# Kernel tuning notes

Measured on AMD Instinct MI355X. Metric: run time of the kernel, lower is better.

## Reference

```python
import jax, jax.numpy as jnp
import numpy as np

B, S, H = 32, 2048, 1024


def setup_inputs() -> dict:
    key = jax.random.key(0)
    k1, k2, k3, k4, k5, k6 = jax.random.split(key, 6)
    hidden = jax.random.normal(k1, (B, H), dtype=jnp.float32)
    encoder_outputs = jax.random.normal(k2, (B, S, H), dtype=jnp.float32)
    lengths = jax.random.randint(k3, (B,), 1, S + 1, dtype=jnp.int64)
    scale = 1.0 / np.sqrt(H)
    Wq = jax.random.normal(k4, (H, H), dtype=jnp.float32) * scale
    Wk = jax.random.normal(k5, (H, H), dtype=jnp.float32) * scale
    v = jax.random.uniform(k6, (H,), dtype=jnp.float32)  # torch.rand init
    return {"hidden": hidden, "encoder_outputs": encoder_outputs,
            "lengths": lengths, "Wq": Wq, "Wk": Wk, "v": v}


def reference(hidden, encoder_outputs, lengths, Wq, Wk, v):
    # query: (B, 1, H); nn.Linear(bias=False) applies x @ W.T
    query = (hidden @ Wq.T)[:, None, :]
    keys = jnp.einsum('bsh,kh->bsk', encoder_outputs, Wk)  # (B, S, H)
    energy = jnp.tanh(query + keys)                         # (B, S, H)
    attn = jnp.einsum('bsh,h->bs', energy, v)               # (B, S)
    seq = encoder_outputs.shape[1]
    mask = jnp.arange(seq)[None, :] < lengths[:, None]      # (B, S)
    attn = jnp.where(mask, attn, -jnp.inf)
    return jax.nn.softmax(attn, axis=1)
```

## Files before the change

kernel.cpp:

```cpp
#include <hip/hip_runtime.h>
#include <hip/hip_fp16.h>
#include <stdint.h>

#define B_SZ 32
#define S_SZ 2048
#define H_SZ 1024
#define M_SZ (B_SZ * S_SZ)

typedef _Float16 half8 __attribute__((ext_vector_type(8)));
typedef float floatx4 __attribute__((ext_vector_type(4)));

struct h4 { _Float16 x, y, z, w; };

__global__ __launch_bounds__(256) void convert_f32_to_f16(
    const float* __restrict__ in, h4* __restrict__ out, int n4) {
  int i = blockIdx.x * blockDim.x + threadIdx.x;
  int stride = gridDim.x * blockDim.x;
  const float4* in4 = (const float4*)in;
  for (; i < n4; i += stride) {
    float4 f = in4[i];
    h4 o;
    o.x = (_Float16)f.x; o.y = (_Float16)f.y;
    o.z = (_Float16)f.z; o.w = (_Float16)f.w;
    out[i] = o;
  }
}

__global__ __launch_bounds__(256) void query_kernel(
    const float* __restrict__ hidden, const float* __restrict__ Wq,
    float* __restrict__ q) {
  int t = blockIdx.x * blockDim.x + threadIdx.x;
  int b = t & 31;
  int n = t >> 5;
  const float4* h4p = (const float4*)(hidden + (size_t)b * H_SZ);
  const float4* w4p = (const float4*)(Wq + (size_t)n * H_SZ);
  float acc = 0.f;
  #pragma unroll 4
  for (int i = 0; i < H_SZ / 4; ++i) {
    float4 h = h4p[i], w = w4p[i];
    acc = fmaf(h.x, w.x, acc);
    acc = fmaf(h.y, w.y, acc);
    acc = fmaf(h.z, w.z, acc);
    acc = fmaf(h.w, w.w, acc);
  }
  q[(size_t)b * H_SZ + n] = acc;
}

__device__ __forceinline__ void gl_lds16(const void* g, void* l) {
  __builtin_amdgcn_global_load_lds(
      (const __attribute__((address_space(1))) void*)g,
      (__attribute__((address_space(3))) void*)l,
      16, 0, 0);
}

__device__ __forceinline__ float fast_tanh(float x) {
  float ax = fabsf(x);
  float e = __expf(ax * -2.0f);
  float t = (1.0f - e) / (1.0f + e);
  return copysignf(t, x);
}

#define TILE 128
#define BK 32

__global__ __launch_bounds__(256) void fused_keys_kernel(
    const _Float16* __restrict__ A,
    const _Float16* __restrict__ Bt,
    const float* __restrict__ q,
    const float* __restrict__ v,
    float* __restrict__ partial)
{
  __shared__ _Float16 As[TILE * BK];
  __shared__ _Float16 Bs[TILE * BK];
  __shared__ float rowsum[TILE];
  __shared__ float q_l[TILE];
  __shared__ float v_l[TILE];

  const int tid  = threadIdx.x;
  const int w    = tid >> 6;
  const int lane = tid & 63;
  const int bm   = blockIdx.x >> 3;
  const int bn   = blockIdx.x & 7;
  const int R0   = bm * TILE;
  const int C0   = bn * TILE;
  const int bidx = R0 >> 11;

  if (tid < TILE) {
    q_l[tid] = q[(size_t)bidx * H_SZ + C0 + tid];
    v_l[tid] = v[C0 + tid];
    rowsum[tid] = 0.f;
  }

  const int wm = w >> 1, wn = w & 1;
  const int cL = lane & 15, quad = lane >> 4;

  floatx4 acc[4][4];
  #pragma unroll
  for (int m = 0; m < 4; ++m)
    #pragma unroll
    for (int n = 0; n < 4; ++n)
      acc[m][n] = (floatx4){0.f, 0.f, 0.f, 0.f};

  const int srow   = lane >> 2;
  const int schunk = lane & 3;

  const _Float16* Ablk = A + (size_t)R0 * H_SZ;
  const _Float16* Bblk = Bt + (size_t)C0 * H_SZ;

  for (int kt = 0; kt < H_SZ / BK; ++kt) {
    __syncthreads();
    const int kof = kt * BK;
    #pragma unroll
    for (int r = 0; r < 2; ++r) {
      const int row = w * 16 + r * 64 + srow;
      const int ldsbase = (w * 16 + r * 64) * (BK * 2);
      gl_lds16(Ablk + (size_t)row * H_SZ + kof + schunk * 8, (char*)As + ldsbase);
      gl_lds16(Bblk + (size_t)row * H_SZ + kof + schunk * 8, (char*)Bs + ldsbase);
    }
    __syncthreads();

    half8 af[4], bf[4];
    #pragma unroll
    for (int m = 0; m < 4; ++m)
      af[m] = *(const half8*)(As + (wm * 64 + m * 16 + cL) * BK + quad * 8);
    #pragma unroll
    for (int n = 0; n < 4; ++n)
      bf[n] = *(const half8*)(Bs + (wn * 64 + n * 16 + cL) * BK + quad * 8);
    #pragma unroll
    for (int m = 0; m < 4; ++m)
      #pragma unroll
      for (int n = 0; n < 4; ++n)
        acc[m][n] = __builtin_amdgcn_mfma_f32_16x16x32_f16(af[m], bf[n], acc[m][n], 0, 0, 0);
  }

  float qv[4], vv[4];
  #pragma unroll
  for (int n = 0; n < 4; ++n) {
    const int col = wn * 64 + n * 16 + cL;
    qv[n] = q_l[col];
    vv[n] = v_l[col];
  }
  #pragma unroll
  for (int m = 0; m < 4; ++m) {
    #pragma unroll
    for (int r = 0; r < 4; ++r) {
      float s = 0.f;
      #pragma unroll
      for (int n = 0; n < 4; ++n)
        s += vv[n] * fast_tanh(qv[n] + acc[m][n][r]);
      s += __shfl_xor(s, 1);
      s += __shfl_xor(s, 2);
      s += __shfl_xor(s, 4);
      s += __shfl_xor(s, 8);
      if (cL == 0)
        atomicAdd(&rowsum[wm * 64 + m * 16 + quad * 4 + r], s);
    }
  }
  __syncthreads();
  if (tid < TILE)
    partial[(size_t)bn * M_SZ + R0 + tid] = rowsum[tid];
}

__global__ __launch_bounds__(256) void softmax_kernel(
    const float* __restrict__ partial, const int* __restrict__ lengths,
    float* __restrict__ out) {
  __shared__ float wred[4];
  __shared__ float wsum[4];
  const int b = blockIdx.x;
  const int tid = threadIdx.x;
  const int len = lengths[b];

  float lg[8];
  #pragma unroll
  for (int i = 0; i < 8; ++i) {
    const int s = tid + i * 256;
    const size_t row = (size_t)b * S_SZ + s;
    float l = 0.f;
    #pragma unroll
    for (int nt = 0; nt < 8; ++nt) l += partial[(size_t)nt * M_SZ + row];
    lg[i] = (s < len) ? l : -INFINITY;
  }

  float mx = lg[0];
  #pragma unroll
  for (int i = 1; i < 8; ++i) mx = fmaxf(mx, lg[i]);
  #pragma unroll
  for (int off = 32; off; off >>= 1) mx = fmaxf(mx, __shfl_xor(mx, off));
  if ((tid & 63) == 0) wred[tid >> 6] = mx;
  __syncthreads();
  mx = fmaxf(fmaxf(wred[0], wred[1]), fmaxf(wred[2], wred[3]));

  float pe[8];
  float sum = 0.f;
  #pragma unroll
  for (int i = 0; i < 8; ++i) {
    float e = (lg[i] == -INFINITY) ? 0.f : __expf(lg[i] - mx);
    pe[i] = e;
    sum += e;
  }
  #pragma unroll
  for (int off = 32; off; off >>= 1) sum += __shfl_xor(sum, off);
  if ((tid & 63) == 0) wsum[tid >> 6] = sum;
  __syncthreads();
  sum = wsum[0] + wsum[1] + wsum[2] + wsum[3];
  const float inv = 1.0f / sum;

  #pragma unroll
  for (int i = 0; i < 8; ++i) {
    const int s = tid + i * 256;
    out[(size_t)b * S_SZ + s] = pe[i] * inv;
  }
}

extern "C" void kernel_launch(void* const* d_in, const int* in_sizes, int n_in,
                              void* d_out, int out_size, void* d_ws, size_t ws_size,
                              hipStream_t stream) {
  const float* hidden  = (const float*)d_in[0];
  const float* enc     = (const float*)d_in[1];
  const int*   lengths = (const int*)d_in[2];
  const float* Wq      = (const float*)d_in[3];
  const float* Wk      = (const float*)d_in[4];
  const float* v       = (const float*)d_in[5];
  float* out = (float*)d_out;

  char* ws = (char*)d_ws;
  _Float16* A16     = (_Float16*)ws;
  _Float16* B16     = (_Float16*)(ws + 134217728);
  float*    q       = (float*)(ws + 134217728 + 2097152);
  float*    partial = (float*)(ws + 134217728 + 2097152 + 131072);

  convert_f32_to_f16<<<8192, 256, 0, stream>>>(enc, (h4*)A16, (M_SZ * H_SZ) / 4);
  convert_f32_to_f16<<<1024, 256, 0, stream>>>(Wk, (h4*)B16, (H_SZ * H_SZ) / 4);
  query_kernel<<<128, 256, 0, stream>>>(hidden, Wq, q);
  fused_keys_kernel<<<(M_SZ / TILE) * (H_SZ / TILE), 256, 0, stream>>>(A16, B16, q, v, partial);
  softmax_kernel<<<B_SZ, 256, 0, stream>>>(partial, lengths, out);
}
```

Measured before the change: 627.2 us.

## Fuse encoder fp32-to-fp16 conversion into GEMM tile loads, remap blocks, parallelize query

Drops the separate pass that converted the whole encoder tensor to fp16. The GEMM now loads fp32 tiles straight into LDS in an MFMA-fragment-friendly layout and converts to fp16 when reading fragments, which removes a full read and write of the large activation tensor. The block index is remapped so the eight column tiles of a group of row tiles run close together, to improve L2 reuse of A. The query GEMV now uses one wavefront per output with a shuffle reduction. In exchange, A tiles take twice the LDS space and global bandwidth inside the GEMM, and every block pays conversion work in its inner loop.

```diff
diff --git a/kernel.cpp b/kernel.cpp
--- a/kernel.cpp
+++ b/kernel.cpp
@@ -29,21 +29,25 @@
 __global__ __launch_bounds__(256) void query_kernel(
     const float* __restrict__ hidden, const float* __restrict__ Wq,
     float* __restrict__ q) {
-  int t = blockIdx.x * blockDim.x + threadIdx.x;
-  int b = t & 31;
-  int n = t >> 5;
-  const float4* h4p = (const float4*)(hidden + (size_t)b * H_SZ);
-  const float4* w4p = (const float4*)(Wq + (size_t)n * H_SZ);
+  const int W = blockIdx.x * 4 + (threadIdx.x >> 6);
+  const int lane = threadIdx.x & 63;
+  const int b = W >> 10;
+  const int n = W & 1023;
+  const float4* hp = (const float4*)(hidden + (size_t)b * H_SZ);
+  const float4* wp = (const float4*)(Wq + (size_t)n * H_SZ);
   float acc = 0.f;
-  #pragma unroll 4
-  for (int i = 0; i < H_SZ / 4; ++i) {
-    float4 h = h4p[i], w = w4p[i];
+  #pragma unroll
+  for (int i = 0; i < 4; ++i) {
+    float4 h = hp[lane + 64 * i];
+    float4 w = wp[lane + 64 * i];
     acc = fmaf(h.x, w.x, acc);
     acc = fmaf(h.y, w.y, acc);
     acc = fmaf(h.z, w.z, acc);
     acc = fmaf(h.w, w.w, acc);
   }
-  q[(size_t)b * H_SZ + n] = acc;
+  #pragma unroll
+  for (int off = 32; off; off >>= 1) acc += __shfl_xor(acc, off);
+  if (lane == 0) q[(size_t)b * H_SZ + n] = acc;
 }
 
 __device__ __forceinline__ void gl_lds16(const void* g, void* l) {
@@ -64,13 +68,13 @@
 #define BK 32
 
 __global__ __launch_bounds__(256) void fused_keys_kernel(
-    const _Float16* __restrict__ A,
+    const float* __restrict__ A,
     const _Float16* __restrict__ Bt,
     const float* __restrict__ q,
     const float* __restrict__ v,
     float* __restrict__ partial)
 {
-  __shared__ _Float16 As[TILE * BK];
+  __shared__ float    As[TILE * BK];
   __shared__ _Float16 Bs[TILE * BK];
   __shared__ float rowsum[TILE];
   __shared__ float q_l[TILE];
@@ -79,10 +83,11 @@
   const int tid  = threadIdx.x;
   const int w    = tid >> 6;
   const int lane = tid & 63;
-  const int bm   = blockIdx.x >> 3;
-  const int bn   = blockIdx.x & 7;
-  const int R0   = bm * TILE;
-  const int C0   = bn * TILE;
+
+  const int bm = ((blockIdx.x >> 6) << 3) | (blockIdx.x & 7);
+  const int bn = (blockIdx.x >> 3) & 7;
+  const int R0 = bm * TILE;
+  const int C0 = bn * TILE;
   const int bidx = R0 >> 11;
 
   if (tid < TILE) {
@@ -101,31 +106,53 @@
     for (int n = 0; n < 4; ++n)
       acc[m][n] = (floatx4){0.f, 0.f, 0.f, 0.f};
 
-  const int srow   = lane >> 2;
-  const int schunk = lane & 3;
-
-  const _Float16* Ablk = A + (size_t)R0 * H_SZ;
-  const _Float16* Bblk = Bt + (size_t)C0 * H_SZ;
+  const float* pA[4];
+  #pragma unroll
+  for (int i = 0; i < 4; ++i) {
+    const int j = w * 4 + i;
+    const int row = ((j >> 3) * 64) + (((j >> 1) & 3) * 16) + cL;
+    const int kf  = quad * 8 + (j & 1) * 4;
+    pA[i] = A + (size_t)(R0 + row) * H_SZ + kf;
+  }
+  const _Float16* pB[2];
+  #pragma unroll
+  for (int i = 0; i < 2; ++i) {
+    const int j = w + 4 * i;
+    const int row = ((j >> 2) * 64) + ((j & 3) * 16) + cL;
+    pB[i] = Bt + (size_t)(C0 + row) * H_SZ + quad * 8;
+  }
 
   for (int kt = 0; kt < H_SZ / BK; ++kt) {
     __syncthreads();
-    const int kof = kt * BK;
-    #pragma unroll
-    for (int r = 0; r < 2; ++r) {
-      const int row = w * 16 + r * 64 + srow;
-      const int ldsbase = (w * 16 + r * 64) * (BK * 2);
-      gl_lds16(Ablk + (size_t)row * H_SZ + kof + schunk * 8, (char*)As + ldsbase);
-      gl_lds16(Bblk + (size_t)row * H_SZ + kof + schunk * 8, (char*)Bs + ldsbase);
+    #pragma unroll
+    for (int i = 0; i < 4; ++i) {
+      const int j = w * 4 + i;
+      gl_lds16(pA[i], (char*)As + j * 1024);
+      pA[i] += BK;
+    }
+    #pragma unroll
+    for (int i = 0; i < 2; ++i) {
+      const int j = w + 4 * i;
+      gl_lds16(pB[i], (char*)Bs + j * 1024);
+      pB[i] += BK;
     }
     __syncthreads();
 
     half8 af[4], bf[4];
     #pragma unroll
-    for (int m = 0; m < 4; ++m)
-      af[m] = *(const half8*)(As + (wm * 64 + m * 16 + cL) * BK + quad * 8);
+    for (int m = 0; m < 4; ++m) {
+      float4 lo = *(const float4*)((const char*)As + wm * 8192 + m * 2048 + lane * 16);
+      float4 hi = *(const float4*)((const char*)As + wm * 8192 + m * 2048 + 1024 + lane * 16);
+      half8 a;
+      a[0] = (_Float16)lo.x; a[1] = (_Float16)lo.y;
+      a[2] = (_Float16)lo.z; a[3] = (_Float16)lo.w;
+      a[4] = (_Float16)hi.x; a[5] = (_Float16)hi.y;
+      a[6] = (_Float16)hi.z; a[7] = (_Float16)hi.w;
+      af[m] = a;
+    }
     #pragma unroll
     for (int n = 0; n < 4; ++n)
-      bf[n] = *(const half8*)(Bs + (wn * 64 + n * 16 + cL) * BK + quad * 8);
+      bf[n] = *(const half8*)((const char*)Bs + wn * 4096 + n * 1024 + lane * 16);
     #pragma unroll
     for (int m = 0; m < 4; ++m)
       #pragma unroll
@@ -224,14 +251,12 @@
   float* out = (float*)d_out;
 
   char* ws = (char*)d_ws;
-  _Float16* A16     = (_Float16*)ws;
-  _Float16* B16     = (_Float16*)(ws + 134217728);
-  float*    q       = (float*)(ws + 134217728 + 2097152);
-  float*    partial = (float*)(ws + 134217728 + 2097152 + 131072);
-
-  convert_f32_to_f16<<<8192, 256, 0, stream>>>(enc, (h4*)A16, (M_SZ * H_SZ) / 4);
+  _Float16* B16     = (_Float16*)ws;
+  float*    q       = (float*)(ws + 2097152);
+  float*    partial = (float*)(ws + 2097152 + 131072);
+
   convert_f32_to_f16<<<1024, 256, 0, stream>>>(Wk, (h4*)B16, (H_SZ * H_SZ) / 4);
-  query_kernel<<<128, 256, 0, stream>>>(hidden, Wq, q);
-  fused_keys_kernel<<<(M_SZ / TILE) * (H_SZ / TILE), 256, 0, stream>>>(A16, B16, q, v, partial);
+  query_kernel<<<8192, 256, 0, stream>>>(hidden, Wq, q);
+  fused_keys_kernel<<<(M_SZ / TILE) * (H_SZ / TILE), 256, 0, stream>>>(enc, B16, q, v, partial);
   softmax_kernel<<<B_SZ, 256, 0, stream>>>(partial, lengths, out);
 }
```

Measured after the change: 694.4 us. 1.11x slower.
